# Optimization experiments

Measured on AMD Instinct MI355X. Metric: run time of the kernel, lower is better.

## Reference

```python
import jax, jax.numpy as jnp
import numpy as np

N, K, D = 131072, 2048, 512


def setup_inputs() -> dict:
    key = jax.random.key(0)
    kx, kc = jax.random.split(key)
    x = jax.random.normal(kx, (N, D), dtype=jnp.float32)
    cluster_centers = jax.random.normal(kc, (K, D), dtype=jnp.float32)
    return {"x": x, "cluster_centers": cluster_centers}


def reference(x, cluster_centers):
    # d_{nk} = ||x_n - c_k||_2; argmin over k.
    x2 = jnp.sum(x * x, axis=-1, keepdims=True)            # [N,1]
    c2 = jnp.sum(cluster_centers * cluster_centers, -1)    # [K]
    d2 = x2 + c2 - 2.0 * (x @ cluster_centers.T)           # [N,K]
    # sqrt is monotonic, so argmin over squared distances equals argmin over L2 norms
    return jnp.argmin(d2, axis=-1)                          # [N] int
```

## Files before the change

### kernel.cpp

```cpp
#include <hip/hip_runtime.h>


#define N_PTS 131072
#define K_CL  2048
#define D_DIM 512
#define BM 128
#define BN 128
#define BK 32
#define NKT (K_CL / BN)
#define NDT (D_DIM / BK)
#define NT  (NKT * NDT)

typedef _Float16 half8  __attribute__((ext_vector_type(8)));
typedef _Float16 half4v __attribute__((ext_vector_type(4)));
typedef float    floatx4 __attribute__((ext_vector_type(4)));

#define GLL(g, l) __builtin_amdgcn_global_load_lds( \
    (__attribute__((address_space(1))) void*)(g),   \
    (__attribute__((address_space(3))) void*)(l), 16, 0, 0)

__global__ void row_norms_kernel(const float* __restrict__ A,
                                 float* __restrict__ out, int rows) {
    int gid  = blockIdx.x * blockDim.x + threadIdx.x;
    int wave = gid >> 6;
    int lane = gid & 63;
    if (wave >= rows) return;
    const float4* a = (const float4*)(A + (size_t)wave * D_DIM);
    float4 p = a[lane];
    float4 q = a[lane + 64];
    float s = p.x*p.x + p.y*p.y + p.z*p.z + p.w*p.w
            + q.x*q.x + q.y*q.y + q.z*q.z + q.w*q.w;
    #pragma unroll
    for (int off = 32; off > 0; off >>= 1) s += __shfl_down(s, off, 64);
    if (lane == 0) out[wave] = s;
}

__global__ void conv_f16x2_kernel(const float* __restrict__ src,
                                  _Float16* __restrict__ hi,
                                  _Float16* __restrict__ lo, int n4) {
    int i = blockIdx.x * blockDim.x + threadIdx.x;
    if (i >= n4) return;
    float4 v = ((const float4*)src)[i];
    half4v h, l;
    h.x = (_Float16)v.x; h.y = (_Float16)v.y;
    h.z = (_Float16)v.z; h.w = (_Float16)v.w;
    l.x = (_Float16)(v.x - (float)h.x);
    l.y = (_Float16)(v.y - (float)h.y);
    l.z = (_Float16)(v.z - (float)h.z);
    l.w = (_Float16)(v.w - (float)h.w);
    *(half4v*)(hi + (size_t)i * 4) = h;
    *(half4v*)(lo + (size_t)i * 4) = l;
}

template<bool XPRE, bool CPRE>
__global__ __launch_bounds__(256, 2)
void kmeans_mfma(const float* __restrict__ X, const float* __restrict__ C,
                 const _Float16* __restrict__ Xhi, const _Float16* __restrict__ Xlo,
                 const _Float16* __restrict__ Chi, const _Float16* __restrict__ Clo,
                 const float* __restrict__ c2g, int* __restrict__ out) {
    constexpr bool ASYNC = XPRE && CPRE;

    __shared__ __align__(16) _Float16 sXh[2][BM * BK], sXl[2][BM * BK];
    __shared__ __align__(16) _Float16 sCh[2][BN * BK], sCl[2][BN * BK];
    __shared__ float c2s[K_CL];
    __shared__ float x2s[BM];

    const int tid  = threadIdx.x;
    const int lane = tid & 63;
    const int w    = tid >> 6;
    const int wti  = w >> 1;
    const int wtj  = w & 1;
    const int q    = lane >> 4;
    const int m16  = lane & 15;
    const int rowBase = blockIdx.x * BM;

    const int jsrc = (((lane & 3) ^ ((lane >> 3) & 3)) * 8);
    const int swq8 = ((q ^ ((m16 >> 1) & 3)) * 8);

    if (CPRE) {
        for (int i = tid; i < K_CL / 4; i += 256)
            ((float4*)c2s)[i] = ((const float4*)c2g)[i];
    } else {
        for (int k = tid; k < K_CL; k += 256) {
            const float4* cp = (const float4*)(C + (size_t)k * D_DIM);
            float s0 = 0.f, s1 = 0.f;
            for (int j = 0; j < D_DIM / 4; j += 2) {
                float4 a = cp[j], b = cp[j + 1];
                s0 += a.x*a.x + a.y*a.y + a.z*a.z + a.w*a.w;
                s1 += b.x*b.x + b.y*b.y + b.z*b.z + b.w*b.w;
            }
            c2s[k] = s0 + s1;
        }
    }
    {
        int r = tid & 127, h = tid >> 7;
        const float4* xp = (const float4*)(X + (size_t)(rowBase + r) * D_DIM + h * 256);
        float s0 = 0.f, s1 = 0.f;
        for (int j = 0; j < 64; j += 2) {
            float4 a = xp[j], b = xp[j + 1];
            s0 += a.x*a.x + a.y*a.y + a.z*a.z + a.w*a.w;
            s1 += b.x*b.x + b.y*b.y + b.z*b.z + b.w*b.w;
        }
        ((float*)sXh)[tid] = s0 + s1;
    }
    __syncthreads();
    if (tid < BM) x2s[tid] = ((float*)sXh)[tid] + ((float*)sXh)[tid + 128];
    __syncthreads();

    const int s_c4 = tid & 7;
    const int s_r0 = tid >> 3;

    auto stage = [&](int t) {
        const int dtl = t & (NDT - 1);
        const int ktl = t >> 4;
        const int d0  = dtl * BK;
        const int k0l = ktl * BN;
        const int b   = t & 1;
        _Float16* dXh = sXh[b]; _Float16* dXl = sXl[b];
        _Float16* dCh = sCh[b]; _Float16* dCl = sCl[b];
        if constexpr (XPRE) {
            #pragma unroll
            for (int s = 0; s < 2; ++s) {
                const int cc = w * 2 + s;
                const int r  = cc * 16 + (lane >> 2);
                const size_t go = (size_t)(rowBase + r) * D_DIM + d0 + jsrc;
                GLL(Xhi + go, &dXh[cc * 512]);
                GLL(Xlo + go, &dXl[cc * 512]);
            }
        } else {
            #pragma unroll
            for (int p = 0; p < 4; ++p) {
                const int r = s_r0 + p * 32;
                float4 v = *(const float4*)&X[(size_t)(rowBase + r) * D_DIM + d0 + s_c4 * 4];
                half4v h, l;
                h.x = (_Float16)v.x; h.y = (_Float16)v.y;
                h.z = (_Float16)v.z; h.w = (_Float16)v.w;
                l.x = (_Float16)(v.x - (float)h.x);
                l.y = (_Float16)(v.y - (float)h.y);
                l.z = (_Float16)(v.z - (float)h.z);
                l.w = (_Float16)(v.w - (float)h.w);
                const int off = r * BK + (((s_c4 >> 1) ^ ((r >> 1) & 3)) * 8) + (s_c4 & 1) * 4;
                *(half4v*)&dXh[off] = h;
                *(half4v*)&dXl[off] = l;
            }
        }
        if constexpr (CPRE) {
            #pragma unroll
            for (int s = 0; s < 2; ++s) {
                const int cc = w * 2 + s;
                const int r  = cc * 16 + (lane >> 2);
                const size_t go = (size_t)(k0l + r) * D_DIM + d0 + jsrc;
                GLL(Chi + go, &dCh[cc * 512]);
                GLL(Clo + go, &dCl[cc * 512]);
            }
        } else {
            #pragma unroll
            for (int p = 0; p < 4; ++p) {
                const int r = s_r0 + p * 32;
                float4 v = *(const float4*)&C[(size_t)(k0l + r) * D_DIM + d0 + s_c4 * 4];
                half4v h, l;
                h.x = (_Float16)v.x; h.y = (_Float16)v.y;
                h.z = (_Float16)v.z; h.w = (_Float16)v.w;
                l.x = (_Float16)(v.x - (float)h.x);
                l.y = (_Float16)(v.y - (float)h.y);
                l.z = (_Float16)(v.z - (float)h.z);
                l.w = (_Float16)(v.w - (float)h.w);
                const int off = r * BK + (((s_c4 >> 1) ^ ((r >> 1) & 3)) * 8) + (s_c4 & 1) * 4;
                *(half4v*)&dCh[off] = h;
                *(half4v*)&dCl[off] = l;
            }
        }
    };

    float bestV[4][4];
    int   bestI[4][4];
    #pragma unroll
    for (int ti = 0; ti < 4; ++ti)
        #pragma unroll
        for (int r = 0; r < 4; ++r) { bestV[ti][r] = 3.4e38f; bestI[ti][r] = 0; }

    stage(0);
    stage(1);
    if constexpr (ASYNC) {
        asm volatile("s_waitcnt vmcnt(8)" ::: "memory");
        __builtin_amdgcn_s_barrier();
    } else {
        __syncthreads();
    }

    #pragma unroll 1
    for (int kt = 0; kt < NKT; ++kt) {
        const int k0 = kt * BN;
        floatx4 acc[4][4];
        #pragma unroll
        for (int ti = 0; ti < 4; ++ti)
            #pragma unroll
            for (int tj = 0; tj < 4; ++tj) acc[ti][tj] = (floatx4){0.f, 0.f, 0.f, 0.f};

        #pragma unroll 2
        for (int dt = 0; dt < NDT; ++dt) {
            const int t = kt * NDT + dt;
            const int b = t & 1;
            const _Float16* bXh = sXh[b]; const _Float16* bXl = sXl[b];
            const _Float16* bCh = sCh[b]; const _Float16* bCl = sCl[b];

            half8 ah[4], al[4], bh[4], bl[4];
            #pragma unroll
            for (int ti = 0; ti < 4; ++ti) {
                const int row = wti * 64 + ti * 16 + m16;
                ah[ti] = *(const half8*)&bXh[row * BK + swq8];
                al[ti] = *(const half8*)&bXl[row * BK + swq8];
            }
            #pragma unroll
            for (int tj = 0; tj < 4; ++tj) {
                const int col = wtj * 64 + tj * 16 + m16;
                bh[tj] = *(const half8*)&bCh[col * BK + swq8];
                bl[tj] = *(const half8*)&bCl[col * BK + swq8];
            }

            if constexpr (ASYNC) {
                asm volatile("s_waitcnt lgkmcnt(0)" ::: "memory");
                __builtin_amdgcn_sched_barrier(0);
                __builtin_amdgcn_s_barrier();
            } else {
                __syncthreads();
            }

            if (t + 2 < NT) stage(t + 2);

            __builtin_amdgcn_s_setprio(1);
            #pragma unroll
            for (int tj = 0; tj < 4; ++tj) {
                #pragma unroll
                for (int ti = 0; ti < 4; ++ti) {
                    floatx4 a = acc[ti][tj];
                    a = __builtin_amdgcn_mfma_f32_16x16x32_f16(ah[ti], bh[tj], a, 0, 0, 0);
                    a = __builtin_amdgcn_mfma_f32_16x16x32_f16(ah[ti], bl[tj], a, 0, 0, 0);
                    a = __builtin_amdgcn_mfma_f32_16x16x32_f16(al[ti], bh[tj], a, 0, 0, 0);
                    acc[ti][tj] = a;
                }
            }
            __builtin_amdgcn_s_setprio(0);

            if constexpr (ASYNC) {
                if (t + 2 < NT) asm volatile("s_waitcnt vmcnt(8)" ::: "memory");
                else            asm volatile("s_waitcnt vmcnt(0)" ::: "memory");
                __builtin_amdgcn_s_barrier();
            } else {
                __syncthreads();
            }
        }

        #pragma unroll
        for (int tj = 0; tj < 4; ++tj) {
            int col = k0 + wtj * 64 + tj * 16 + m16;
            float cv = c2s[col];
            #pragma unroll
            for (int ti = 0; ti < 4; ++ti)
                #pragma unroll
                for (int r = 0; r < 4; ++r) {
                    float s = x2s[wti * 64 + ti * 16 + q * 4 + r] + cv;
                    float v = s - 2.0f * acc[ti][tj][r];
                    if (v < bestV[ti][r]) { bestV[ti][r] = v; bestI[ti][r] = col; }
                }
        }
    }

    #pragma unroll
    for (int ti = 0; ti < 4; ++ti)
        #pragma unroll
        for (int r = 0; r < 4; ++r) {
            float v = bestV[ti][r]; int ix = bestI[ti][r];
            #pragma unroll
            for (int off = 1; off < 16; off <<= 1) {
                float ov = __shfl_xor(v, off, 64);
                int   oi = __shfl_xor(ix, off, 64);
                if (ov < v || (ov == v && oi < ix)) { v = ov; ix = oi; }
            }
            bestV[ti][r] = v; bestI[ti][r] = ix;
        }

    __syncthreads();
    float* rv  = (float*)sXh;
    int*   rix = (int*)sCh;
    if (m16 == 0) {
        #pragma unroll
        for (int ti = 0; ti < 4; ++ti)
            #pragma unroll
            for (int r = 0; r < 4; ++r) {
                int rloc = wti * 64 + ti * 16 + q * 4 + r;
                rv[rloc * 2 + wtj]  = bestV[ti][r];
                rix[rloc * 2 + wtj] = bestI[ti][r];
            }
    }
    __syncthreads();
    if (tid < BM) {
        float v0 = rv[tid * 2], v1 = rv[tid * 2 + 1];
        int   i0 = rix[tid * 2], i1 = rix[tid * 2 + 1];
        out[rowBase + tid] = (v1 < v0 || (v1 == v0 && i1 < i0)) ? i1 : i0;
    }
}

extern "C" void kernel_launch(void* const* d_in, const int* in_sizes, int n_in,
                              void* d_out, int out_size, void* d_ws, size_t ws_size,
                              hipStream_t stream) {
    const float* X = (const float*)d_in[0];
    const float* C = (const float*)d_in[1];
    int* out = (int*)d_out;

    char* ws = (char*)d_ws;
    const size_t c2_off  = 0;
    const size_t chi_off = (size_t)K_CL * 4;
    const size_t clo_off = chi_off + (size_t)K_CL * D_DIM * 2;
    const size_t xhi_off = clo_off + (size_t)K_CL * D_DIM * 2;
    const size_t xlo_off = xhi_off + (size_t)N_PTS * D_DIM * 2;
    const size_t need_C    = xhi_off;
    const size_t need_full = xlo_off + (size_t)N_PTS * D_DIM * 2;

    if (ws_size >= need_full) {
        float*    c2  = (float*)(ws + c2_off);
        _Float16* Chi = (_Float16*)(ws + chi_off);
        _Float16* Clo = (_Float16*)(ws + clo_off);
        _Float16* Xhi = (_Float16*)(ws + xhi_off);
        _Float16* Xlo = (_Float16*)(ws + xlo_off);
        row_norms_kernel<<<(K_CL * 64) / 256, 256, 0, stream>>>(C, c2, K_CL);
        conv_f16x2_kernel<<<(K_CL * D_DIM / 4) / 256, 256, 0, stream>>>(
            C, Chi, Clo, K_CL * D_DIM / 4);
        conv_f16x2_kernel<<<(N_PTS * D_DIM / 4 + 255) / 256, 256, 0, stream>>>(
            X, Xhi, Xlo, N_PTS * D_DIM / 4);
        kmeans_mfma<true, true><<<N_PTS / BM, 256, 0, stream>>>(
            X, C, Xhi, Xlo, Chi, Clo, c2, out);
    } else if (ws_size >= need_C) {
        float*    c2  = (float*)(ws + c2_off);
        _Float16* Chi = (_Float16*)(ws + chi_off);
        _Float16* Clo = (_Float16*)(ws + clo_off);
        row_norms_kernel<<<(K_CL * 64) / 256, 256, 0, stream>>>(C, c2, K_CL);
        conv_f16x2_kernel<<<(K_CL * D_DIM / 4) / 256, 256, 0, stream>>>(
            C, Chi, Clo, K_CL * D_DIM / 4);
        kmeans_mfma<false, true><<<N_PTS / BM, 256, 0, stream>>>(
            X, C, nullptr, nullptr, Chi, Clo, c2, out);
    } else {
        kmeans_mfma<false, false><<<N_PTS / BM, 256, 0, stream>>>(
            X, C, nullptr, nullptr, nullptr, nullptr, nullptr, out);
    }
}
```

Baseline: 1.215 ms.

## Interleave LDS fragment loads with MFMA quadrants in the async main loop

Splits the per-k-step LDS fragment reads into four phases, loading only the A/B fragments needed for each 2x2 quadrant of MFMA cells and issuing those MFMAs before the next loads. The aim is to overlap LDS read latency with matrix-core work and reduce register pressure from holding all fragments at once. The global prefetch stage is moved before the last quadrant. This adds several extra workgroup barriers per iteration, which could cost more than the overlap gains.

New measurement: 1.233 ms. About the same (+1.5%).

```diff
diff --git a/kernel.cpp b/kernel.cpp
--- a/kernel.cpp
+++ b/kernel.cpp
@@ -205,50 +205,95 @@
             const _Float16* bCh = sCh[b]; const _Float16* bCl = sCl[b];
 
             half8 ah[4], al[4], bh[4], bl[4];
-            #pragma unroll
-            for (int ti = 0; ti < 4; ++ti) {
-                const int row = wti * 64 + ti * 16 + m16;
-                ah[ti] = *(const half8*)&bXh[row * BK + swq8];
-                al[ti] = *(const half8*)&bXl[row * BK + swq8];
-            }
-            #pragma unroll
-            for (int tj = 0; tj < 4; ++tj) {
-                const int col = wtj * 64 + tj * 16 + m16;
-                bh[tj] = *(const half8*)&bCh[col * BK + swq8];
-                bl[tj] = *(const half8*)&bCl[col * BK + swq8];
-            }
+
+            #define CELL(ti, tj) do {                                              \
+                floatx4 a_ = acc[ti][tj];                                          \
+                a_ = __builtin_amdgcn_mfma_f32_16x16x32_f16(ah[ti], bh[tj], a_, 0, 0, 0); \
+                a_ = __builtin_amdgcn_mfma_f32_16x16x32_f16(ah[ti], bl[tj], a_, 0, 0, 0); \
+                a_ = __builtin_amdgcn_mfma_f32_16x16x32_f16(al[ti], bh[tj], a_, 0, 0, 0); \
+                acc[ti][tj] = a_;                                                  \
+            } while (0)
 
             if constexpr (ASYNC) {
+                #pragma unroll
+                for (int ti = 0; ti < 2; ++ti) {
+                    const int row = wti * 64 + ti * 16 + m16;
+                    ah[ti] = *(const half8*)&bXh[row * BK + swq8];
+                    al[ti] = *(const half8*)&bXl[row * BK + swq8];
+                }
+                #pragma unroll
+                for (int tj = 0; tj < 2; ++tj) {
+                    const int col = wtj * 64 + tj * 16 + m16;
+                    bh[tj] = *(const half8*)&bCh[col * BK + swq8];
+                    bl[tj] = *(const half8*)&bCl[col * BK + swq8];
+                }
+                __builtin_amdgcn_s_barrier();
                 asm volatile("s_waitcnt lgkmcnt(0)" ::: "memory");
                 __builtin_amdgcn_sched_barrier(0);
-                __builtin_amdgcn_s_barrier();
-            } else {
-                __syncthreads();
-            }
-
-            if (t + 2 < NT) stage(t + 2);
-
-            __builtin_amdgcn_s_setprio(1);
-            #pragma unroll
-            for (int tj = 0; tj < 4; ++tj) {
-                #pragma unroll
-                for (int ti = 0; ti < 4; ++ti) {
-                    floatx4 a = acc[ti][tj];
-                    a = __builtin_amdgcn_mfma_f32_16x16x32_f16(ah[ti], bh[tj], a, 0, 0, 0);
-                    a = __builtin_amdgcn_mfma_f32_16x16x32_f16(ah[ti], bl[tj], a, 0, 0, 0);
-                    a = __builtin_amdgcn_mfma_f32_16x16x32_f16(al[ti], bh[tj], a, 0, 0, 0);
-                    acc[ti][tj] = a;
-                }
-            }
-            __builtin_amdgcn_s_setprio(0);
-
-            if constexpr (ASYNC) {
+                __builtin_amdgcn_s_setprio(1);
+                CELL(0, 0); CELL(1, 1); CELL(0, 1); CELL(1, 0);
+                __builtin_amdgcn_s_setprio(0);
+                __builtin_amdgcn_s_barrier();
+
+                #pragma unroll
+                for (int tj = 2; tj < 4; ++tj) {
+                    const int col = wtj * 64 + tj * 16 + m16;
+                    bh[tj] = *(const half8*)&bCh[col * BK + swq8];
+                    bl[tj] = *(const half8*)&bCl[col * BK + swq8];
+                }
+                __builtin_amdgcn_s_barrier();
+                asm volatile("s_waitcnt lgkmcnt(0)" ::: "memory");
+                __builtin_amdgcn_sched_barrier(0);
+                __builtin_amdgcn_s_setprio(1);
+                CELL(0, 2); CELL(1, 3); CELL(0, 3); CELL(1, 2);
+                __builtin_amdgcn_s_setprio(0);
+                __builtin_amdgcn_s_barrier();
+
+                #pragma unroll
+                for (int ti = 2; ti < 4; ++ti) {
+                    const int row = wti * 64 + ti * 16 + m16;
+                    ah[ti] = *(const half8*)&bXh[row * BK + swq8];
+                    al[ti] = *(const half8*)&bXl[row * BK + swq8];
+                }
+                __builtin_amdgcn_s_barrier();
+                asm volatile("s_waitcnt lgkmcnt(0)" ::: "memory");
+                __builtin_amdgcn_sched_barrier(0);
+                __builtin_amdgcn_s_setprio(1);
+                CELL(2, 2); CELL(3, 3); CELL(2, 3); CELL(3, 2);
+                __builtin_amdgcn_s_setprio(0);
+                __builtin_amdgcn_s_barrier();
+
+                if (t + 2 < NT) stage(t + 2);
+                __builtin_amdgcn_s_setprio(1);
+                CELL(2, 0); CELL(3, 1); CELL(2, 1); CELL(3, 0);
+                __builtin_amdgcn_s_setprio(0);
                 if (t + 2 < NT) asm volatile("s_waitcnt vmcnt(8)" ::: "memory");
                 else            asm volatile("s_waitcnt vmcnt(0)" ::: "memory");
                 __builtin_amdgcn_s_barrier();
             } else {
+                #pragma unroll
+                for (int ti = 0; ti < 4; ++ti) {
+                    const int row = wti * 64 + ti * 16 + m16;
+                    ah[ti] = *(const half8*)&bXh[row * BK + swq8];
+                    al[ti] = *(const half8*)&bXl[row * BK + swq8];
+                }
+                #pragma unroll
+                for (int tj = 0; tj < 4; ++tj) {
+                    const int col = wtj * 64 + tj * 16 + m16;
+                    bh[tj] = *(const half8*)&bCh[col * BK + swq8];
+                    bl[tj] = *(const half8*)&bCl[col * BK + swq8];
+                }
                 __syncthreads();
-            }
+                if (t + 2 < NT) stage(t + 2);
+                __builtin_amdgcn_s_setprio(1);
+                #pragma unroll
+                for (int tj = 0; tj < 4; ++tj)
+                    #pragma unroll
+                    for (int ti = 0; ti < 4; ++ti) CELL(ti, tj);
+                __builtin_amdgcn_s_setprio(0);
+                __syncthreads();
+            }
+            #undef CELL
         }
 
         #pragma unroll
```

## Triple-buffer LDS staging to drop one barrier per K-step in async path

Applied to the files above, without the earlier changes.

Moves the async (pre-split fp16 hi/lo) path from double to triple LDS buffering with rotating read/stage indices. The stage for tile t+2 can then be issued without the mid-iteration barrier that guarded buffer reuse, leaving one barrier per step. The c2 norms are now read from global memory instead of being copied into LDS, which frees shared memory for the third buffer. The non-async fallback becomes a simple single-buffer loop. The trade-off is more LDS per block, which could lower occupancy, plus global c2 loads in the epilogue.

After: 1.598 ms. 1.32x slower.

```diff
diff --git a/kernel.cpp b/kernel.cpp
--- a/kernel.cpp
+++ b/kernel.cpp
@@ -59,10 +59,11 @@
                  const _Float16* __restrict__ Chi, const _Float16* __restrict__ Clo,
                  const float* __restrict__ c2g, int* __restrict__ out) {
     constexpr bool ASYNC = XPRE && CPRE;
-
-    __shared__ __align__(16) _Float16 sXh[2][BM * BK], sXl[2][BM * BK];
-    __shared__ __align__(16) _Float16 sCh[2][BN * BK], sCl[2][BN * BK];
-    __shared__ float c2s[K_CL];
+    constexpr int  NB    = ASYNC ? 3 : 2;
+
+    __shared__ __align__(16) _Float16 sXh[NB][BM * BK], sXl[NB][BM * BK];
+    __shared__ __align__(16) _Float16 sCh[NB][BN * BK], sCl[NB][BN * BK];
+    __shared__ float c2s[CPRE ? 1 : K_CL];
     __shared__ float x2s[BM];
 
     const int tid  = threadIdx.x;
@@ -77,10 +78,7 @@
     const int jsrc = (((lane & 3) ^ ((lane >> 3) & 3)) * 8);
     const int swq8 = ((q ^ ((m16 >> 1) & 3)) * 8);
 
-    if (CPRE) {
-        for (int i = tid; i < K_CL / 4; i += 256)
-            ((float4*)c2s)[i] = ((const float4*)c2g)[i];
-    } else {
+    if constexpr (!CPRE) {
         for (int k = tid; k < K_CL; k += 256) {
             const float4* cp = (const float4*)(C + (size_t)k * D_DIM);
             float s0 = 0.f, s1 = 0.f;
@@ -110,12 +108,11 @@
     const int s_c4 = tid & 7;
     const int s_r0 = tid >> 3;
 
-    auto stage = [&](int t) {
+    auto stage = [&](int t, int b) {
         const int dtl = t & (NDT - 1);
         const int ktl = t >> 4;
         const int d0  = dtl * BK;
         const int k0l = ktl * BN;
-        const int b   = t & 1;
         _Float16* dXh = sXh[b]; _Float16* dXl = sXl[b];
         _Float16* dCh = sCh[b]; _Float16* dCl = sCl[b];
         if constexpr (XPRE) {
@@ -179,13 +176,12 @@
         #pragma unroll
         for (int r = 0; r < 4; ++r) { bestV[ti][r] = 3.4e38f; bestI[ti][r] = 0; }
 
-    stage(0);
-    stage(1);
+    int bR = 0, bS = 2;
     if constexpr (ASYNC) {
+        stage(0, 0);
+        stage(1, 1);
         asm volatile("s_waitcnt vmcnt(8)" ::: "memory");
         __builtin_amdgcn_s_barrier();
-    } else {
-        __syncthreads();
     }
 
     #pragma unroll 1
@@ -197,64 +193,81 @@
             #pragma unroll
             for (int tj = 0; tj < 4; ++tj) acc[ti][tj] = (floatx4){0.f, 0.f, 0.f, 0.f};
 
-        #pragma unroll 2
-        for (int dt = 0; dt < NDT; ++dt) {
-            const int t = kt * NDT + dt;
-            const int b = t & 1;
-            const _Float16* bXh = sXh[b]; const _Float16* bXl = sXl[b];
-            const _Float16* bCh = sCh[b]; const _Float16* bCl = sCl[b];
-
-            half8 ah[4], al[4], bh[4], bl[4];
-            #pragma unroll
-            for (int ti = 0; ti < 4; ++ti) {
-                const int row = wti * 64 + ti * 16 + m16;
-                ah[ti] = *(const half8*)&bXh[row * BK + swq8];
-                al[ti] = *(const half8*)&bXl[row * BK + swq8];
-            }
-            #pragma unroll
-            for (int tj = 0; tj < 4; ++tj) {
-                const int col = wtj * 64 + tj * 16 + m16;
-                bh[tj] = *(const half8*)&bCh[col * BK + swq8];
-                bl[tj] = *(const half8*)&bCl[col * BK + swq8];
-            }
-
-            if constexpr (ASYNC) {
-                asm volatile("s_waitcnt lgkmcnt(0)" ::: "memory");
-                __builtin_amdgcn_sched_barrier(0);
-                __builtin_amdgcn_s_barrier();
-            } else {
-                __syncthreads();
-            }
-
-            if (t + 2 < NT) stage(t + 2);
-
-            __builtin_amdgcn_s_setprio(1);
-            #pragma unroll
-            for (int tj = 0; tj < 4; ++tj) {
+        half8 ah[4], al[4], bh[4], bl[4];
+        #define CELL(ti, tj) do {                                              \
+            floatx4 a_ = acc[ti][tj];                                          \
+            a_ = __builtin_amdgcn_mfma_f32_16x16x32_f16(ah[ti], bh[tj], a_, 0, 0, 0); \
+            a_ = __builtin_amdgcn_mfma_f32_16x16x32_f16(ah[ti], bl[tj], a_, 0, 0, 0); \
+            a_ = __builtin_amdgcn_mfma_f32_16x16x32_f16(al[ti], bh[tj], a_, 0, 0, 0); \
+            acc[ti][tj] = a_;                                                  \
+        } while (0)
+
+        if constexpr (ASYNC) {
+            #pragma unroll 2
+            for (int dt = 0; dt < NDT; ++dt) {
+                const int t = kt * NDT + dt;
+                const _Float16* bXh = sXh[bR]; const _Float16* bXl = sXl[bR];
+                const _Float16* bCh = sCh[bR]; const _Float16* bCl = sCl[bR];
+
                 #pragma unroll
                 for (int ti = 0; ti < 4; ++ti) {
-                    floatx4 a = acc[ti][tj];
-                    a = __builtin_amdgcn_mfma_f32_16x16x32_f16(ah[ti], bh[tj], a, 0, 0, 0);
-                    a = __builtin_amdgcn_mfma_f32_16x16x32_f16(ah[ti], bl[tj], a, 0, 0, 0);
-                    a = __builtin_amdgcn_mfma_f32_16x16x32_f16(al[ti], bh[tj], a, 0, 0, 0);
-                    acc[ti][tj] = a;
-                }
-            }
-            __builtin_amdgcn_s_setprio(0);
-
-            if constexpr (ASYNC) {
+                    const int row = wti * 64 + ti * 16 + m16;
+                    ah[ti] = *(const half8*)&bXh[row * BK + swq8];
+                    al[ti] = *(const half8*)&bXl[row * BK + swq8];
+                }
+                #pragma unroll
+                for (int tj = 0; tj < 4; ++tj) {
+                    const int col = wtj * 64 + tj * 16 + m16;
+                    bh[tj] = *(const half8*)&bCh[col * BK + swq8];
+                    bl[tj] = *(const half8*)&bCl[col * BK + swq8];
+                }
+
+                if (t + 2 < NT) stage(t + 2, bS);
+
+                __builtin_amdgcn_s_setprio(1);
+                #pragma unroll
+                for (int tj = 0; tj < 4; ++tj)
+                    #pragma unroll
+                    for (int ti = 0; ti < 4; ++ti) CELL(ti, tj);
+                __builtin_amdgcn_s_setprio(0);
+
                 if (t + 2 < NT) asm volatile("s_waitcnt vmcnt(8)" ::: "memory");
                 else            asm volatile("s_waitcnt vmcnt(0)" ::: "memory");
                 __builtin_amdgcn_s_barrier();
-            } else {
+                bR = (bR == NB - 1) ? 0 : bR + 1;
+                bS = (bS == NB - 1) ? 0 : bS + 1;
+            }
+        } else {
+            #pragma unroll 1
+            for (int dt = 0; dt < NDT; ++dt) {
+                const int t = kt * NDT + dt;
                 __syncthreads();
-            }
-        }
+                stage(t, 0);
+                __syncthreads();
+                #pragma unroll
+                for (int ti = 0; ti < 4; ++ti) {
+                    const int row = wti * 64 + ti * 16 + m16;
+                    ah[ti] = *(const half8*)&sXh[0][row * BK + swq8];
+                    al[ti] = *(const half8*)&sXl[0][row * BK + swq8];
+                }
+                #pragma unroll
+                for (int tj = 0; tj < 4; ++tj) {
+                    const int col = wtj * 64 + tj * 16 + m16;
+                    bh[tj] = *(const half8*)&sCh[0][col * BK + swq8];
+                    bl[tj] = *(const half8*)&sCl[0][col * BK + swq8];
+                }
+                #pragma unroll
+                for (int tj = 0; tj < 4; ++tj)
+                    #pragma unroll
+                    for (int ti = 0; ti < 4; ++ti) CELL(ti, tj);
+            }
+        }
+        #undef CELL
 
         #pragma unroll
         for (int tj = 0; tj < 4; ++tj) {
             int col = k0 + wtj * 64 + tj * 16 + m16;
-            float cv = c2s[col];
+            float cv = CPRE ? c2g[col] : c2s[col];
             #pragma unroll
             for (int ti = 0; ti < 4; ++ti)
                 #pragma unroll
```
